# Kernel optimization log

Measured on AMD Instinct MI355X. Metric: run time of the kernel, lower is better.

The kernel has to match this reference:

```python
import jax, jax.numpy as jnp
import numpy as np

N = 131072   # n_agents
K = 2        # k_neighbors = k_obstacles
H, C = 4, 128
HC = H * C   # 512
OBS_DIM = 37
OUT = 4


def setup_inputs() -> dict:
    key = jax.random.key(0)
    ks = jax.random.split(key, 40)
    s = 0.05
    def g(i, shape):
        return jax.random.normal(ks[i], shape, dtype=jnp.float32) * s
    inp = {"obs": jax.random.normal(ks[0], (N, OBS_DIM), dtype=jnp.float32)}
    # layer 0 (query_dim = 19)
    inp["wq0"] = g(1, (19, HC)); inp["wak0"] = g(2, (6, HC)); inp["wav0"] = g(3, (7, HC))
    inp["wok0"] = g(4, (2, HC)); inp["wov0"] = g(5, (2, HC))
    inp["apw0"] = g(6, (HC, C)); inp["apb0"] = jnp.zeros((C,), jnp.float32)
    inp["opw0"] = g(7, (HC, C)); inp["opb0"] = jnp.zeros((C,), jnp.float32)
    inp["fpw0"] = g(8, (2 * C, C)); inp["fpb0"] = jnp.zeros((C,), jnp.float32)
    inp["ca0"] = jnp.float32(1.0); inp["co0"] = jnp.float32(2.0)
    # layer 1 (query_dim = gnn_hidden_dim = 128)
    inp["wq1"] = g(9, (C, HC)); inp["wak1"] = g(10, (6, HC)); inp["wav1"] = g(11, (7, HC))
    inp["wok1"] = g(12, (2, HC)); inp["wov1"] = g(13, (2, HC))
    inp["apw1"] = g(14, (HC, C)); inp["apb1"] = jnp.zeros((C,), jnp.float32)
    inp["opw1"] = g(15, (HC, C)); inp["opb1"] = jnp.zeros((C,), jnp.float32)
    inp["fpw1"] = g(16, (2 * C, C)); inp["fpb1"] = jnp.zeros((C,), jnp.float32)
    inp["ca1"] = jnp.float32(1.0); inp["co1"] = jnp.float32(2.0)
    # output head
    inp["headw"] = g(17, (C, OUT)); inp["headb"] = jnp.zeros((OUT,), jnp.float32)
    return inp


def _forward(obs, wq0, wak0, wav0, wok0, wov0, apw0, apb0, opw0, opb0, fpw0, fpb0, ca0, co0,
             wq1, wak1, wav1, wok1, wov1, apw1, apb1, opw1, opb1, fpw1, fpb1, ca1, co1,
             headw, headb):
    n = obs.shape[0]
    scale = (C // H) ** -0.5  # matches torch: (out_channels // heads) ** -0.5

    # feature extraction per ObservationConfig (k=2)
    qf = jnp.concatenate([obs[:, 0:12], obs[:, 30:37]], axis=-1)        # [n, 19]
    nb = obs[:, 12:24].reshape(n, K, 6)                                  # neighbor keys [n,k,6]
    nbv = jnp.concatenate([nb, obs[:, 24:26][..., None]], axis=-1)       # + progress -> [n,k,7]
    ob = obs[:, 26:30].reshape(n, K, 2)                                  # obstacle k/v [n,k,2]
    apos = obs[:, 0:2]
    npos = nb[..., 0:2]
    opos = ob

    def attend(q, kfeat, vfeat, wk, wv, pw, pb, decay, pos_k):
        keys = (kfeat @ wk).reshape(n, K, H, C)
        vals = (vfeat @ wv).reshape(n, K, H, C)
        dist = jnp.linalg.norm(apos[:, None, :] - pos_k, axis=-1)        # [n,k]
        dw = jnp.exp(-decay * dist)                                      # [n,k]
        dot = jnp.einsum('nhc,nkhc->nhk', q, keys) * scale
        att = jax.nn.softmax(dot * dw[:, None, :], axis=-1)
        out = jnp.einsum('nhk,nkhc->nhc', att, vals).reshape(n, HC)
        return out @ pw + pb                                             # [n, C]

    def layer(qfeat, wq, wak, wav, wok, wov, apw, apb, opw, opb, fpw, fpb, ca, co):
        q = (qfeat @ wq).reshape(n, H, C)
        a = attend(q, nb, nbv, wak, wav, apw, apb, ca, npos)
        o = attend(q, ob, ob, wok, wov, opw, opb, co, opos)
        return jnp.concatenate([a, o], axis=-1) @ fpw + fpb              # [n, C]

    h = layer(qf, wq0, wak0, wav0, wok0, wov0, apw0, apb0, opw0, opb0, fpw0, fpb0, ca0, co0)
    h = layer(h, wq1, wak1, wav1, wok1, wov1, apw1, apb1, opw1, opb1, fpw1, fpb1, ca1, co1)
    return h @ headw + headb                                             # [n, OUT]


def reference(obs, wq0, wak0, wav0, wok0, wov0, apw0, apb0, opw0, opb0, fpw0, fpb0, ca0, co0,
              wq1, wak1, wav1, wok1, wov1, apw1, apb1, opw1, opb1, fpw1, fpb1, ca1, co1,
              headw, headb):
    return _forward(obs, wq0, wak0, wav0, wok0, wov0, apw0, apb0, opw0, opb0, fpw0, fpb0, ca0, co0,
                    wq1, wak1, wav1, wok1, wov1, apw1, apb1, opw1, opb1, fpw1, fpb1, ca1, co1,
                    headw, headb)
```

## Files before the change

kernel.cpp:

```cpp
#include <hip/hip_runtime.h>
#include <math.h>

#define NTH 256

typedef float v4f __attribute__((ext_vector_type(4)));

enum : int {
  WQ0_OFF = 0,
  M_OFF   = 608,
  TB_OFF  = 1760,
  AO1_OFF = 1792,
  B1H_OFF = 1936,
  TBL_N   = 1940,
  WQ1_OFF = 1952,
  PA0_OFF = 6048,
  PO0_OFF = 9632,
  PA1_OFF = 10656,
  PO1_OFF = 14240,
  F1T_OFF = 15264,
  F1B_OFF = 15776,
  B0_OFF  = 16288,
  BB1_OFF = 16416,
  WS_END  = 16544
};

__global__ void prep1(
    const float* __restrict__ wq0, const float* __restrict__ wak0, const float* __restrict__ wok0,
    const float* __restrict__ wq1, const float* __restrict__ wak1, const float* __restrict__ wok1,
    const float* __restrict__ wav0, const float* __restrict__ apw0,
    const float* __restrict__ wov0, const float* __restrict__ opw0,
    const float* __restrict__ wav1, const float* __restrict__ apw1,
    const float* __restrict__ wov1, const float* __restrict__ opw1,
    const float* __restrict__ fpw1, const float* __restrict__ headw,
    const float* __restrict__ fpw0,
    const float* __restrict__ fpb0, const float* __restrict__ apb0, const float* __restrict__ opb0,
    const float* __restrict__ fpb1, const float* __restrict__ apb1, const float* __restrict__ opb1,
    float* __restrict__ ws)
{
  int gid = blockIdx.x * NTH + threadIdx.x;
  if (gid < 608) {
    int j = gid & 7, r = (gid >> 3) % 19, h = gid / 152;
    const float* a = wq0 + r * 512 + h * 128;
    const float* b = ((j < 6) ? (wak0 + j * 512) : (wok0 + (j - 6) * 512)) + h * 128;
    float acc = 0.f;
    for (int c = 0; c < 128; c++) acc += a[c] * b[c];
    ws[WQ0_OFF + gid] = acc;
  } else if (gid < 4704) {
    int idx = gid - 608;
    int j = idx & 7, cc = (idx >> 3) & 127, h = idx >> 10;
    const float* a = wq1 + cc * 512 + h * 128;
    const float* b = ((j < 6) ? (wak1 + j * 512) : (wok1 + (j - 6) * 512)) + h * 128;
    float acc = 0.f;
    for (int c = 0; c < 128; c++) acc += a[c] * b[c];
    ws[WQ1_OFF + idx] = acc;
  } else if (gid < 8288) {
    int idx = gid - 4704;
    int t = idx & 127, i = (idx >> 7) % 7, h = idx / 896;
    const float* w = wav0 + i * 512 + h * 128;
    const float* p = apw0 + (h * 128) * 128 + t;
    float acc = 0.f;
    for (int c = 0; c < 128; c++) acc += w[c] * p[c * 128];
    ws[PA0_OFF + idx] = acc;
  } else if (gid < 9312) {
    int idx = gid - 8288;
    int t = idx & 127, i = (idx >> 7) & 1, h = idx >> 8;
    const float* w = wov0 + i * 512 + h * 128;
    const float* p = opw0 + (h * 128) * 128 + t;
    float acc = 0.f;
    for (int c = 0; c < 128; c++) acc += w[c] * p[c * 128];
    ws[PO0_OFF + idx] = acc;
  } else if (gid < 12896) {
    int idx = gid - 9312;
    int t = idx & 127, i = (idx >> 7) % 7, h = idx / 896;
    const float* w = wav1 + i * 512 + h * 128;
    const float* p = apw1 + (h * 128) * 128 + t;
    float acc = 0.f;
    for (int c = 0; c < 128; c++) acc += w[c] * p[c * 128];
    ws[PA1_OFF + idx] = acc;
  } else if (gid < 13920) {
    int idx = gid - 12896;
    int t = idx & 127, i = (idx >> 7) & 1, h = idx >> 8;
    const float* w = wov1 + i * 512 + h * 128;
    const float* p = opw1 + (h * 128) * 128 + t;
    float acc = 0.f;
    for (int c = 0; c < 128; c++) acc += w[c] * p[c * 128];
    ws[PO1_OFF + idx] = acc;
  } else if (gid < 14432) {
    int idx = gid - 13920;
    int o2 = idx & 3, i = idx >> 2;
    float acc = 0.f;
    for (int j = 0; j < 128; j++) acc += fpw1[i * 128 + j] * headw[j * 4 + o2];
    ws[F1T_OFF + idx] = acc;
  } else if (gid < 14944) {
    int idx = gid - 14432;
    int o2 = idx & 3, i = idx >> 2;
    float acc = 0.f;
    for (int j = 0; j < 128; j++) acc += fpw1[(128 + i) * 128 + j] * headw[j * 4 + o2];
    ws[F1B_OFF + idx] = acc;
  } else if (gid < 15072) {
    int j = gid - 14944;
    float acc = fpb0[j];
    for (int c = 0; c < 128; c++)
      acc += apb0[c] * fpw0[c * 128 + j] + opb0[c] * fpw0[(128 + c) * 128 + j];
    ws[B0_OFF + j] = acc;
  } else if (gid < 15200) {
    int j = gid - 15072;
    float acc = fpb1[j];
    for (int c = 0; c < 128; c++)
      acc += apb1[c] * fpw1[c * 128 + j] + opb1[c] * fpw1[(128 + c) * 128 + j];
    ws[BB1_OFF + j] = acc;
  }
}

__global__ __launch_bounds__(NTH) void prep_late(
    const float* __restrict__ fpw0, const float* __restrict__ headw,
    const float* __restrict__ headb, float* __restrict__ ws)
{
  const int b = blockIdx.x;
  const int tid = threadIdx.x;
  if (b < 36) {
    __shared__ float sAO0[128];
    const int t = b, h = t / 9, i = t % 9;
    if (tid < 128) {
      float acc = 0.f;
      if (i < 7) {
        const float* P = ws + PA0_OFF + (h * 7 + i) * 128;
        for (int u = 0; u < 128; u++) acc += P[u] * fpw0[u * 128 + tid];
      } else {
        const float* P = ws + PO0_OFF + (h * 2 + (i - 7)) * 128;
        for (int u = 0; u < 128; u++) acc += P[u] * fpw0[(128 + u) * 128 + tid];
      }
      sAO0[tid] = acc;
    }
    __syncthreads();
    if (tid < 32) {
      const int h2 = tid >> 3, j2 = tid & 7;
      float acc = 0.f;
      const float* W = ws + WQ1_OFF + h2 * 1024 + j2;
      for (int c = 0; c < 128; c++) acc += sAO0[c] * W[c * 8];
      ws[M_OFF + t * 32 + tid] = acc;
    }
  } else {
    if (tid < 144) {
      const int o2 = tid & 3, i = (tid >> 2) % 9, h = tid / 36;
      float acc = 0.f;
      if (i < 7) {
        const float* P = ws + PA1_OFF + (h * 7 + i) * 128;
        for (int u = 0; u < 128; u++) acc += P[u] * ws[F1T_OFF + u * 4 + o2];
      } else {
        const float* P = ws + PO1_OFF + (h * 2 + (i - 7)) * 128;
        for (int u = 0; u < 128; u++) acc += P[u] * ws[F1B_OFF + u * 4 + o2];
      }
      ws[AO1_OFF + tid] = acc;
    } else if (tid < 176) {
      const int idx = tid - 144;
      const int j = idx & 7, h = idx >> 3;
      float acc = 0.f;
      for (int cc = 0; cc < 128; cc++)
        acc += ws[B0_OFF + cc] * ws[WQ1_OFF + h * 1024 + cc * 8 + j];
      ws[TB_OFF + idx] = acc;
    } else if (tid < 180) {
      const int o2 = tid - 176;
      float acc = headb[o2];
      for (int j = 0; j < 128; j++) acc += ws[BB1_OFF + j] * headw[j * 4 + o2];
      ws[B1H_OFF + o2] = acc;
    }
  }
}

__global__ __launch_bounds__(NTH) void actor_main(
    const float* __restrict__ obs, const float* __restrict__ ws,
    const float* __restrict__ pca0, const float* __restrict__ pco0,
    const float* __restrict__ pca1, const float* __restrict__ pco1,
    float* __restrict__ out, int n)
{
  const int gid = blockIdx.x * NTH + threadIdx.x;
  if (gid >= n) return;

  const v4f* __restrict__ tbl = (const v4f*)ws;

  float o[37];
  {
    const float* op = obs + (size_t)gid * 37;
#pragma unroll
    for (int i = 0; i < 37; i++) o[i] = op[i];
  }
  const float scale = 0.17677669529663687f;

  float qf[19];
#pragma unroll
  for (int i = 0; i < 12; i++) qf[i] = o[i];
#pragma unroll
  for (int i = 0; i < 7; i++) qf[12 + i] = o[30 + i];
  float nb[2][6];
#pragma unroll
  for (int k2 = 0; k2 < 2; k2++)
#pragma unroll
    for (int i = 0; i < 6; i++) nb[k2][i] = o[12 + 6 * k2 + i];
  const float nbv6[2] = { o[24], o[25] };
  const float obf[2][2] = { { o[26], o[27] }, { o[28], o[29] } };
  const float ax = o[0], ay = o[1];

  float dista[2], disto[2];
#pragma unroll
  for (int k2 = 0; k2 < 2; k2++) {
    float dx = ax - nb[k2][0], dy = ay - nb[k2][1];
    dista[k2] = sqrtf(dx * dx + dy * dy);
    float ex = ax - obf[k2][0], ey = ay - obf[k2][1];
    disto[k2] = sqrtf(ex * ex + ey * ey);
  }
  const float ca0 = pca0[0], co0 = pco0[0], ca1 = pca1[0], co1 = pco1[0];
  float dwa0[2], dwo0[2], dwa1[2], dwo1[2];
#pragma unroll
  for (int k2 = 0; k2 < 2; k2++) {
    dwa0[k2] = __expf(-ca0 * dista[k2]);
    dwo0[k2] = __expf(-co0 * disto[k2]);
    dwa1[k2] = __expf(-ca1 * dista[k2]);
    dwo1[k2] = __expf(-co1 * disto[k2]);
  }

  v4f t0v[8];
#pragma unroll
  for (int z = 0; z < 8; z++) t0v[z] = (v4f)0.f;
#pragma unroll
  for (int h = 0; h < 4; h++) {
#pragma unroll
    for (int r = 0; r < 19; r++) {
      float q = qf[r];
      t0v[h * 2 + 0] += tbl[(h * 19 + r) * 2 + 0] * q;
      t0v[h * 2 + 1] += tbl[(h * 19 + r) * 2 + 1] * q;
    }
  }

  float wff[36];
#pragma unroll
  for (int h = 0; h < 4; h++) {
    float la[2], lo[2];
#pragma unroll
    for (int k2 = 0; k2 < 2; k2++) {
      float da = t0v[h*2][0]*nb[k2][0] + t0v[h*2][1]*nb[k2][1] + t0v[h*2][2]*nb[k2][2]
               + t0v[h*2][3]*nb[k2][3] + t0v[h*2+1][0]*nb[k2][4] + t0v[h*2+1][1]*nb[k2][5];
      la[k2] = da * scale * dwa0[k2];
      float dof = t0v[h*2+1][2]*obf[k2][0] + t0v[h*2+1][3]*obf[k2][1];
      lo[k2] = dof * scale * dwo0[k2];
    }
    float e  = __expf(la[1] - la[0]); float aa1 = e  / (1.f + e);  float aa0 = 1.f - aa1;
    float eo = __expf(lo[1] - lo[0]); float bo1 = eo / (1.f + eo); float bo0 = 1.f - bo1;
#pragma unroll
    for (int i = 0; i < 6; i++) wff[h * 9 + i] = aa0 * nb[0][i] + aa1 * nb[1][i];
    wff[h * 9 + 6] = aa0 * nbv6[0] + aa1 * nbv6[1];
    wff[h * 9 + 7] = bo0 * obf[0][0] + bo1 * obf[1][0];
    wff[h * 9 + 8] = bo0 * obf[0][1] + bo1 * obf[1][1];
  }

  v4f t1v[8];
#pragma unroll
  for (int q = 0; q < 8; q++) t1v[q] = tbl[440 + q];
#pragma unroll
  for (int t = 0; t < 36; t++) {
    float f = wff[t];
#pragma unroll
    for (int q = 0; q < 8; q++)
      t1v[q] += tbl[152 + t * 8 + q] * f;
  }

  float wf1f[36];
#pragma unroll
  for (int h = 0; h < 4; h++) {
    float la[2], lo[2];
#pragma unroll
    for (int k2 = 0; k2 < 2; k2++) {
      float da = t1v[h*2][0]*nb[k2][0] + t1v[h*2][1]*nb[k2][1] + t1v[h*2][2]*nb[k2][2]
               + t1v[h*2][3]*nb[k2][3] + t1v[h*2+1][0]*nb[k2][4] + t1v[h*2+1][1]*nb[k2][5];
      la[k2] = da * scale * dwa1[k2];
      float dof = t1v[h*2+1][2]*obf[k2][0] + t1v[h*2+1][3]*obf[k2][1];
      lo[k2] = dof * scale * dwo1[k2];
    }
    float e  = __expf(la[1] - la[0]); float aa1 = e  / (1.f + e);  float aa0 = 1.f - aa1;
    float eo = __expf(lo[1] - lo[0]); float bo1 = eo / (1.f + eo); float bo0 = 1.f - bo1;
#pragma unroll
    for (int i = 0; i < 6; i++) wf1f[h * 9 + i] = aa0 * nb[0][i] + aa1 * nb[1][i];
    wf1f[h * 9 + 6] = aa0 * nbv6[0] + aa1 * nbv6[1];
    wf1f[h * 9 + 7] = bo0 * obf[0][0] + bo1 * obf[1][0];
    wf1f[h * 9 + 8] = bo0 * obf[0][1] + bo1 * obf[1][1];
  }

  v4f acc = tbl[484];
#pragma unroll
  for (int t = 0; t < 36; t++)
    acc += tbl[448 + t] * wf1f[t];
  ((v4f*)out)[gid] = acc;
}

extern "C" void kernel_launch(void* const* d_in, const int* in_sizes, int n_in,
                              void* d_out, int out_size, void* d_ws, size_t ws_size,
                              hipStream_t stream)
{
  const float* obs  = (const float*)d_in[0];
  const float* wq0  = (const float*)d_in[1];
  const float* wak0 = (const float*)d_in[2];
  const float* wav0 = (const float*)d_in[3];
  const float* wok0 = (const float*)d_in[4];
  const float* wov0 = (const float*)d_in[5];
  const float* apw0 = (const float*)d_in[6];
  const float* apb0 = (const float*)d_in[7];
  const float* opw0 = (const float*)d_in[8];
  const float* opb0 = (const float*)d_in[9];
  const float* fpw0 = (const float*)d_in[10];
  const float* fpb0 = (const float*)d_in[11];
  const float* ca0  = (const float*)d_in[12];
  const float* co0  = (const float*)d_in[13];
  const float* wq1  = (const float*)d_in[14];
  const float* wak1 = (const float*)d_in[15];
  const float* wav1 = (const float*)d_in[16];
  const float* wok1 = (const float*)d_in[17];
  const float* wov1 = (const float*)d_in[18];
  const float* apw1 = (const float*)d_in[19];
  const float* apb1 = (const float*)d_in[20];
  const float* opw1 = (const float*)d_in[21];
  const float* opb1 = (const float*)d_in[22];
  const float* fpw1 = (const float*)d_in[23];
  const float* fpb1 = (const float*)d_in[24];
  const float* ca1  = (const float*)d_in[25];
  const float* co1  = (const float*)d_in[26];
  const float* headw = (const float*)d_in[27];
  const float* headb = (const float*)d_in[28];
  float* ws = (float*)d_ws;
  int n = in_sizes[0] / 37;

  prep1<<<(15200 + NTH - 1) / NTH, NTH, 0, stream>>>(
      wq0, wak0, wok0, wq1, wak1, wok1,
      wav0, apw0, wov0, opw0, wav1, apw1, wov1, opw1,
      fpw1, headw, fpw0, fpb0, apb0, opb0, fpb1, apb1, opb1, ws);
  prep_late<<<37, NTH, 0, stream>>>(fpw0, headw, headb, ws);
  actor_main<<<(n + NTH - 1) / NTH, NTH, 0, stream>>>(
      obs, ws, ca0, co0, ca1, co1, (float*)d_out, n);
}
```

Baseline: 167.6 us.

## Fuse weight-prep kernels, stage obs through LDS, and prefetch obs

Merges the two weight-precomputation kernels into one launch whose blocks each compute a chain of small matvecs through shared memory. The attention scale is now folded into the precomputed tables, so it is no longer multiplied per agent. Spare blocks of the prep kernel stride-read the obs array to warm the cache before the main kernel runs. The main kernel loads each block's obs rows with coalesced float4 loads into LDS instead of strided per-thread loads. This trades extra LDS use and a barrier for fewer launches and better global memory coalescing.

New measurement: 174.2 us. 1.04x slower.

```diff
diff --git a/kernel.cpp b/kernel.cpp
--- a/kernel.cpp
+++ b/kernel.cpp
@@ -12,159 +12,154 @@
   AO1_OFF = 1792,
   B1H_OFF = 1936,
   TBL_N   = 1940,
-  WQ1_OFF = 1952,
-  PA0_OFF = 6048,
-  PO0_OFF = 9632,
-  PA1_OFF = 10656,
-  PO1_OFF = 14240,
-  F1T_OFF = 15264,
-  F1B_OFF = 15776,
-  B0_OFF  = 16288,
-  BB1_OFF = 16416,
-  WS_END  = 16544
+  PREF_SCRATCH = 4096
 };
 
-__global__ void prep1(
-    const float* __restrict__ wq0, const float* __restrict__ wak0, const float* __restrict__ wok0,
-    const float* __restrict__ wq1, const float* __restrict__ wak1, const float* __restrict__ wok1,
-    const float* __restrict__ wav0, const float* __restrict__ apw0,
-    const float* __restrict__ wov0, const float* __restrict__ opw0,
-    const float* __restrict__ wav1, const float* __restrict__ apw1,
-    const float* __restrict__ wov1, const float* __restrict__ opw1,
-    const float* __restrict__ fpw1, const float* __restrict__ headw,
-    const float* __restrict__ fpw0,
-    const float* __restrict__ fpb0, const float* __restrict__ apb0, const float* __restrict__ opb0,
-    const float* __restrict__ fpb1, const float* __restrict__ apb1, const float* __restrict__ opb1,
-    float* __restrict__ ws)
-{
-  int gid = blockIdx.x * NTH + threadIdx.x;
-  if (gid < 608) {
-    int j = gid & 7, r = (gid >> 3) % 19, h = gid / 152;
-    const float* a = wq0 + r * 512 + h * 128;
-    const float* b = ((j < 6) ? (wak0 + j * 512) : (wok0 + (j - 6) * 512)) + h * 128;
-    float acc = 0.f;
-    for (int c = 0; c < 128; c++) acc += a[c] * b[c];
-    ws[WQ0_OFF + gid] = acc;
-  } else if (gid < 4704) {
-    int idx = gid - 608;
-    int j = idx & 7, cc = (idx >> 3) & 127, h = idx >> 10;
-    const float* a = wq1 + cc * 512 + h * 128;
-    const float* b = ((j < 6) ? (wak1 + j * 512) : (wok1 + (j - 6) * 512)) + h * 128;
-    float acc = 0.f;
-    for (int c = 0; c < 128; c++) acc += a[c] * b[c];
-    ws[WQ1_OFF + idx] = acc;
-  } else if (gid < 8288) {
-    int idx = gid - 4704;
-    int t = idx & 127, i = (idx >> 7) % 7, h = idx / 896;
-    const float* w = wav0 + i * 512 + h * 128;
-    const float* p = apw0 + (h * 128) * 128 + t;
-    float acc = 0.f;
-    for (int c = 0; c < 128; c++) acc += w[c] * p[c * 128];
-    ws[PA0_OFF + idx] = acc;
-  } else if (gid < 9312) {
-    int idx = gid - 8288;
-    int t = idx & 127, i = (idx >> 7) & 1, h = idx >> 8;
-    const float* w = wov0 + i * 512 + h * 128;
-    const float* p = opw0 + (h * 128) * 128 + t;
-    float acc = 0.f;
-    for (int c = 0; c < 128; c++) acc += w[c] * p[c * 128];
-    ws[PO0_OFF + idx] = acc;
-  } else if (gid < 12896) {
-    int idx = gid - 9312;
-    int t = idx & 127, i = (idx >> 7) % 7, h = idx / 896;
-    const float* w = wav1 + i * 512 + h * 128;
-    const float* p = apw1 + (h * 128) * 128 + t;
-    float acc = 0.f;
-    for (int c = 0; c < 128; c++) acc += w[c] * p[c * 128];
-    ws[PA1_OFF + idx] = acc;
-  } else if (gid < 13920) {
-    int idx = gid - 12896;
-    int t = idx & 127, i = (idx >> 7) & 1, h = idx >> 8;
-    const float* w = wov1 + i * 512 + h * 128;
-    const float* p = opw1 + (h * 128) * 128 + t;
-    float acc = 0.f;
-    for (int c = 0; c < 128; c++) acc += w[c] * p[c * 128];
-    ws[PO1_OFF + idx] = acc;
-  } else if (gid < 14432) {
-    int idx = gid - 13920;
-    int o2 = idx & 3, i = idx >> 2;
-    float acc = 0.f;
-    for (int j = 0; j < 128; j++) acc += fpw1[i * 128 + j] * headw[j * 4 + o2];
-    ws[F1T_OFF + idx] = acc;
-  } else if (gid < 14944) {
-    int idx = gid - 14432;
-    int o2 = idx & 3, i = idx >> 2;
-    float acc = 0.f;
-    for (int j = 0; j < 128; j++) acc += fpw1[(128 + i) * 128 + j] * headw[j * 4 + o2];
-    ws[F1B_OFF + idx] = acc;
-  } else if (gid < 15072) {
-    int j = gid - 14944;
-    float acc = fpb0[j];
-    for (int c = 0; c < 128; c++)
-      acc += apb0[c] * fpw0[c * 128 + j] + opb0[c] * fpw0[(128 + c) * 128 + j];
-    ws[B0_OFF + j] = acc;
-  } else if (gid < 15200) {
-    int j = gid - 15072;
-    float acc = fpb1[j];
-    for (int c = 0; c < 128; c++)
-      acc += apb1[c] * fpw1[c * 128 + j] + opb1[c] * fpw1[(128 + c) * 128 + j];
-    ws[BB1_OFF + j] = acc;
-  }
-}
-
-__global__ __launch_bounds__(NTH) void prep_late(
-    const float* __restrict__ fpw0, const float* __restrict__ headw,
-    const float* __restrict__ headb, float* __restrict__ ws)
+__global__ __launch_bounds__(NTH) void prep_fused(
+    const float* __restrict__ wq0,  const float* __restrict__ wak0, const float* __restrict__ wok0,
+    const float* __restrict__ wav0, const float* __restrict__ wov0,
+    const float* __restrict__ apw0, const float* __restrict__ opw0,
+    const float* __restrict__ fpw0, const float* __restrict__ fpb0,
+    const float* __restrict__ apb0, const float* __restrict__ opb0,
+    const float* __restrict__ wq1,  const float* __restrict__ wak1, const float* __restrict__ wok1,
+    const float* __restrict__ wav1, const float* __restrict__ wov1,
+    const float* __restrict__ apw1, const float* __restrict__ opw1,
+    const float* __restrict__ fpw1, const float* __restrict__ fpb1,
+    const float* __restrict__ apb1, const float* __restrict__ opb1,
+    const float* __restrict__ headw, const float* __restrict__ headb,
+    const float* __restrict__ obs, float* __restrict__ ws, int n)
 {
   const int b = blockIdx.x;
   const int tid = threadIdx.x;
+  const float scale = 0.17677669529663687f;
+  __shared__ float sm[768];
+
   if (b < 36) {
-    __shared__ float sAO0[128];
-    const int t = b, h = t / 9, i = t % 9;
-    if (tid < 128) {
-      float acc = 0.f;
-      if (i < 7) {
-        const float* P = ws + PA0_OFF + (h * 7 + i) * 128;
-        for (int u = 0; u < 128; u++) acc += P[u] * fpw0[u * 128 + tid];
-      } else {
-        const float* P = ws + PO0_OFF + (h * 2 + (i - 7)) * 128;
-        for (int u = 0; u < 128; u++) acc += P[u] * fpw0[(128 + u) * 128 + tid];
-      }
-      sAO0[tid] = acc;
+    const int t = b, h0 = t / 9, i0 = t % 9;
+    float* sP = sm; float* sA = sm + 128; float* sG = sm + 256;
+    if (tid < 128) {
+      const float* w  = (i0 < 7 ? wav0 + i0 * 512 : wov0 + (i0 - 7) * 512) + h0 * 128;
+      const float* pw = (i0 < 7 ? apw0 : opw0) + (h0 * 128) * 128 + tid;
+      float acc = 0.f;
+#pragma unroll 4
+      for (int c = 0; c < 128; c++) acc += w[c] * pw[c * 128];
+      sP[tid] = acc;
+    }
+    __syncthreads();
+    if (tid < 128) {
+      const float* f = fpw0 + (i0 < 7 ? 0 : 128 * 128) + tid;
+      float acc = 0.f;
+#pragma unroll 4
+      for (int u = 0; u < 128; u++) acc += sP[u] * f[u * 128];
+      sA[tid] = acc;
+    }
+    __syncthreads();
+#pragma unroll
+    for (int rep = 0; rep < 2; rep++) {
+      const int hd = tid + rep * 256;
+      float acc = 0.f;
+#pragma unroll 4
+      for (int c = 0; c < 128; c++) acc += sA[c] * wq1[c * 512 + hd];
+      sG[hd] = acc;
     }
     __syncthreads();
     if (tid < 32) {
       const int h2 = tid >> 3, j2 = tid & 7;
-      float acc = 0.f;
-      const float* W = ws + WQ1_OFF + h2 * 1024 + j2;
-      for (int c = 0; c < 128; c++) acc += sAO0[c] * W[c * 8];
-      ws[M_OFF + t * 32 + tid] = acc;
+      const float* wb = (j2 < 6 ? wak1 + j2 * 512 : wok1 + (j2 - 6) * 512) + h2 * 128;
+      const float* g = sG + h2 * 128;
+      float acc = 0.f;
+#pragma unroll 4
+      for (int d = 0; d < 128; d++) acc += g[d] * wb[d];
+      ws[M_OFF + t * 32 + tid] = acc * scale;
+    }
+  } else if (b < 72) {
+    const int t1 = b - 36, h = t1 / 9, i = t1 % 9;
+    float* sP = sm; float* sR = sm + 128;
+    if (tid < 128) {
+      const float* w  = (i < 7 ? wav1 + i * 512 : wov1 + (i - 7) * 512) + h * 128;
+      const float* pw = (i < 7 ? apw1 : opw1) + (h * 128) * 128 + tid;
+      float acc = 0.f;
+#pragma unroll 4
+      for (int c = 0; c < 128; c++) acc += w[c] * pw[c * 128];
+      sP[tid] = acc;
+    }
+    __syncthreads();
+    if (tid < 128) {
+      const float* f = fpw1 + (i < 7 ? 0 : 128 * 128) + tid;
+      float acc = 0.f;
+#pragma unroll 4
+      for (int u = 0; u < 128; u++) acc += sP[u] * f[u * 128];
+      sR[tid] = acc;
+    }
+    __syncthreads();
+    if (tid < 4) {
+      float acc = 0.f;
+#pragma unroll 4
+      for (int j = 0; j < 128; j++) acc += sR[j] * headw[j * 4 + tid];
+      ws[AO1_OFF + t1 * 4 + tid] = acc;
+    }
+  } else if (b == 72) {
+    float* sB = sm; float* sG = sm + 256;
+    if (tid < 128) {
+      float acc = fpb0[tid];
+#pragma unroll 4
+      for (int c = 0; c < 128; c++)
+        acc += apb0[c] * fpw0[c * 128 + tid] + opb0[c] * fpw0[(128 + c) * 128 + tid];
+      sB[tid] = acc;
+    }
+    __syncthreads();
+#pragma unroll
+    for (int rep = 0; rep < 2; rep++) {
+      const int hd = tid + rep * 256;
+      float acc = 0.f;
+#pragma unroll 4
+      for (int cc = 0; cc < 128; cc++) acc += sB[cc] * wq1[cc * 512 + hd];
+      sG[hd] = acc;
+    }
+    __syncthreads();
+    if (tid < 32) {
+      const int h = tid >> 3, j = tid & 7;
+      const float* wb = (j < 6 ? wak1 + j * 512 : wok1 + (j - 6) * 512) + h * 128;
+      const float* g = sG + h * 128;
+      float acc = 0.f;
+#pragma unroll 4
+      for (int d = 0; d < 128; d++) acc += g[d] * wb[d];
+      ws[TB_OFF + tid] = acc * scale;
+    }
+  } else if (b == 73) {
+    float* sB = sm;
+    if (tid < 128) {
+      float acc = fpb1[tid];
+#pragma unroll 4
+      for (int c = 0; c < 128; c++)
+        acc += apb1[c] * fpw1[c * 128 + tid] + opb1[c] * fpw1[(128 + c) * 128 + tid];
+      sB[tid] = acc;
+    }
+    __syncthreads();
+    if (tid < 4) {
+      float acc = headb[tid];
+#pragma unroll 4
+      for (int j = 0; j < 128; j++) acc += sB[j] * headw[j * 4 + tid];
+      ws[B1H_OFF + tid] = acc;
+    }
+  } else if (b < 77) {
+    const int idx = (b - 74) * NTH + tid;
+    if (idx < 608) {
+      const int j = idx & 7, r = (idx >> 3) % 19, h = idx / 152;
+      const v4f* a4 = (const v4f*)(wq0 + r * 512 + h * 128);
+      const v4f* b4 = (const v4f*)((j < 6 ? wak0 + j * 512 : wok0 + (j - 6) * 512) + h * 128);
+      v4f va = (v4f)0.f;
+#pragma unroll 8
+      for (int c = 0; c < 32; c++) va += a4[c] * b4[c];
+      ws[WQ0_OFF + idx] = (va[0] + va[1] + va[2] + va[3]) * scale;
     }
   } else {
-    if (tid < 144) {
-      const int o2 = tid & 3, i = (tid >> 2) % 9, h = tid / 36;
-      float acc = 0.f;
-      if (i < 7) {
-        const float* P = ws + PA1_OFF + (h * 7 + i) * 128;
-        for (int u = 0; u < 128; u++) acc += P[u] * ws[F1T_OFF + u * 4 + o2];
-      } else {
-        const float* P = ws + PO1_OFF + (h * 2 + (i - 7)) * 128;
-        for (int u = 0; u < 128; u++) acc += P[u] * ws[F1B_OFF + u * 4 + o2];
-      }
-      ws[AO1_OFF + tid] = acc;
-    } else if (tid < 176) {
-      const int idx = tid - 144;
-      const int j = idx & 7, h = idx >> 3;
-      float acc = 0.f;
-      for (int cc = 0; cc < 128; cc++)
-        acc += ws[B0_OFF + cc] * ws[WQ1_OFF + h * 1024 + cc * 8 + j];
-      ws[TB_OFF + idx] = acc;
-    } else if (tid < 180) {
-      const int o2 = tid - 176;
-      float acc = headb[o2];
-      for (int j = 0; j < 128; j++) acc += ws[BB1_OFF + j] * headw[j * 4 + o2];
-      ws[B1H_OFF + o2] = acc;
-    }
+    const int pid = (b - 77) * NTH + tid;
+    const size_t total = (size_t)n * 37;
+    float s = 0.f;
+    for (size_t p = (size_t)pid * 32; p < total; p += (size_t)(512 - 77) * NTH * 32)
+      s += obs[p];
+    ws[PREF_SCRATCH + pid] = s;
   }
 }
 
@@ -174,18 +169,49 @@
     const float* __restrict__ pca1, const float* __restrict__ pco1,
     float* __restrict__ out, int n)
 {
-  const int gid = blockIdx.x * NTH + threadIdx.x;
+  const int tid = threadIdx.x;
+  const int gid = blockIdx.x * NTH + tid;
+
+  __shared__ v4f sObsV[NTH * 37 / 4];
+  float* sObs = (float*)sObsV;
+  {
+    const size_t total_f = (size_t)n * 37;
+    const size_t v4base = (size_t)blockIdx.x * (NTH * 37 / 4);
+    const v4f* src = (const v4f*)obs;
+#pragma unroll
+    for (int k = 0; k < 9; k++) {
+      const size_t vi = v4base + k * NTH + tid;
+      if (vi * 4 + 4 <= total_f) {
+        sObsV[k * NTH + tid] = src[vi];
+      } else {
+#pragma unroll
+        for (int e = 0; e < 4; e++) {
+          const size_t f = vi * 4 + e;
+          if (f < total_f) sObs[(k * NTH + tid) * 4 + e] = obs[f];
+        }
+      }
+    }
+    if (tid < 64) {
+      const size_t vi = v4base + 9 * NTH + tid;
+      if (vi * 4 + 4 <= total_f) {
+        sObsV[9 * NTH + tid] = src[vi];
+      } else {
+#pragma unroll
+        for (int e = 0; e < 4; e++) {
+          const size_t f = vi * 4 + e;
+          if (f < total_f) sObs[(9 * NTH + tid) * 4 + e] = obs[f];
+        }
+      }
+    }
+  }
+  __syncthreads();
   if (gid >= n) return;
 
   const v4f* __restrict__ tbl = (const v4f*)ws;
 
   float o[37];
-  {
-    const float* op = obs + (size_t)gid * 37;
-#pragma unroll
-    for (int i = 0; i < 37; i++) o[i] = op[i];
-  }
-  const float scale = 0.17677669529663687f;
+#pragma unroll
+  for (int i = 0; i < 37; i++) o[i] = sObs[tid * 37 + i];
 
   float qf[19];
 #pragma unroll
@@ -240,9 +266,9 @@
     for (int k2 = 0; k2 < 2; k2++) {
       float da = t0v[h*2][0]*nb[k2][0] + t0v[h*2][1]*nb[k2][1] + t0v[h*2][2]*nb[k2][2]
                + t0v[h*2][3]*nb[k2][3] + t0v[h*2+1][0]*nb[k2][4] + t0v[h*2+1][1]*nb[k2][5];
-      la[k2] = da * scale * dwa0[k2];
+      la[k2] = da * dwa0[k2];
       float dof = t0v[h*2+1][2]*obf[k2][0] + t0v[h*2+1][3]*obf[k2][1];
-      lo[k2] = dof * scale * dwo0[k2];
+      lo[k2] = dof * dwo0[k2];
     }
     float e  = __expf(la[1] - la[0]); float aa1 = e  / (1.f + e);  float aa0 = 1.f - aa1;
     float eo = __expf(lo[1] - lo[0]); float bo1 = eo / (1.f + eo); float bo0 = 1.f - bo1;
@@ -272,9 +298,9 @@
     for (int k2 = 0; k2 < 2; k2++) {
       float da = t1v[h*2][0]*nb[k2][0] + t1v[h*2][1]*nb[k2][1] + t1v[h*2][2]*nb[k2][2]
                + t1v[h*2][3]*nb[k2][3] + t1v[h*2+1][0]*nb[k2][4] + t1v[h*2+1][1]*nb[k2][5];
-      la[k2] = da * scale * dwa1[k2];
+      la[k2] = da * dwa1[k2];
       float dof = t1v[h*2+1][2]*obf[k2][0] + t1v[h*2+1][3]*obf[k2][1];
-      lo[k2] = dof * scale * dwo1[k2];
+      lo[k2] = dof * dwo1[k2];
     }
     float e  = __expf(la[1] - la[0]); float aa1 = e  / (1.f + e);  float aa0 = 1.f - aa1;
     float eo = __expf(lo[1] - lo[0]); float bo1 = eo / (1.f + eo); float bo0 = 1.f - bo1;
@@ -328,11 +354,10 @@
   float* ws = (float*)d_ws;
   int n = in_sizes[0] / 37;
 
-  prep1<<<(15200 + NTH - 1) / NTH, NTH, 0, stream>>>(
-      wq0, wak0, wok0, wq1, wak1, wok1,
-      wav0, apw0, wov0, opw0, wav1, apw1, wov1, opw1,
-      fpw1, headw, fpw0, fpb0, apb0, opb0, fpb1, apb1, opb1, ws);
-  prep_late<<<37, NTH, 0, stream>>>(fpw0, headw, headb, ws);
+  prep_fused<<<512, NTH, 0, stream>>>(
+      wq0, wak0, wok0, wav0, wov0, apw0, opw0, fpw0, fpb0, apb0, opb0,
+      wq1, wak1, wok1, wav1, wov1, apw1, opw1, fpw1, fpb1, apb1, opb1,
+      headw, headb, obs, ws, n);
   actor_main<<<(n + NTH - 1) / NTH, NTH, 0, stream>>>(
       obs, ws, ca0, co0, ca1, co1, (float*)d_out, n);
 }
```
